# Performance work log

Measured on AMD Instinct MI355X. Metric: run time of the kernel, lower is better.

The kernel has to match this reference:

```python
import jax, jax.numpy as jnp
import numpy as np

B, S, E, H, NQ = 8, 2048, 8, 2, 8
D = E // H  # head_dim = 4
DIM = 2 ** NQ  # 256-amplitude state vector

# CNOT chain pattern from the module: (0,1),(1,2),...,(NQ-2,NQ-1),(NQ-1,0)
CNOTS = [(i, i + 1) for i in range(NQ - 1)] + [(NQ - 1, 0)]

# Pauli-Z sign table: wire 0 is the most-significant qubit axis (torchquantum convention)
_k = np.arange(DIM)
_SIGNS = (1.0 - 2.0 * ((_k[None, :] >> (NQ - 1 - np.arange(NQ))[:, None]) & 1)).astype(np.float32)  # (NQ, DIM)


def _quantum_measure(tok):
    """Batched simulation of the per-token circuit. tok: (N, E) real -> (N, NQ) <Z> values."""
    n = tok.shape[0]
    idx = jnp.arange(NQ) % D
    # encoder RX(tok[w]) then explicit RX(tok[w % head_dim]) on each wire: angles add.
    half = 0.5 * (tok[:, :NQ] + tok[:, idx])  # (N, NQ)
    a0 = jnp.cos(half).astype(jnp.complex64)
    a1 = (-1j) * jnp.sin(half).astype(jnp.complex64)
    qub = jnp.stack([a0, a1], axis=-1)  # (N, NQ, 2) per-qubit states (product state before CNOTs)
    # Kronecker product across the fixed NQ wires
    state = qub[:, 0, :]
    for w in range(1, NQ):
        state = (state[:, :, None] * qub[:, w, None, :]).reshape(n, -1)
    state = state.reshape((n,) + (2,) * NQ)
    # CNOT chain: flip target axis within control=1 block
    for c, t in CNOTS:
        c0 = jax.lax.index_in_dim(state, 0, c + 1, keepdims=True)
        c1 = jnp.flip(jax.lax.index_in_dim(state, 1, c + 1, keepdims=True), axis=t + 1)
        state = jnp.concatenate([c0, c1], axis=c + 1)
    p = (state.real ** 2 + state.imag ** 2).reshape(n, DIM)  # probabilities
    return p @ jnp.asarray(_SIGNS.T)  # (N, NQ) Pauli-Z expectations


def setup_inputs() -> dict:
    key = jax.random.key(0)
    ks = jax.random.split(key, 5)
    sc = 1.0 / np.sqrt(E)
    return {
        "x": jax.random.normal(ks[0], (B, S, E), jnp.float32),
        "Wq": jax.random.normal(ks[1], (E, E), jnp.float32) * sc,
        "Wk": jax.random.normal(ks[2], (E, E), jnp.float32) * sc,
        "Wv": jax.random.normal(ks[3], (E, E), jnp.float32) * sc,
        "Wo": jax.random.normal(ks[4], (E, E), jnp.float32) * sc,
    }


def reference(x, Wq, Wk, Wv, Wo):
    b, s, _ = x.shape
    # nn.Linear(bias=False): y = x @ W^T
    q = jnp.einsum('bse,fe->bsf', x, Wq).reshape(b, s, H, D)
    k = jnp.einsum('bse,fe->bsf', x, Wk).reshape(b, s, H, D)
    v = jnp.einsum('bse,fe->bsf', x, Wv).reshape(b, s, H, D)
    scores = jnp.einsum('bihd,bjhd->bhij', q, k) / jnp.sqrt(jnp.float32(D))
    attn = jax.nn.softmax(scores, axis=-1)  # dropout is identity at inference
    out = jnp.einsum('bhij,bjhd->bihd', attn, v).reshape(b, s, E)
    z = _quantum_measure(out.reshape(-1, E)).reshape(b, s, NQ)  # NQ == E
    return jnp.einsum('bsq,fq->bsf', z, Wo)
```

## Files before the change

kernel.cpp:

```cpp
#include <hip/hip_runtime.h>


#define SS 2048
#define EE 8

extern "C" __global__ __launch_bounds__(256, 4)
void qa_attn5(const float* __restrict__ x, const float* __restrict__ Wq,
              const float* __restrict__ Wk, const float* __restrict__ Wv,
              float* __restrict__ wsD, float4* __restrict__ wsA) {
    __shared__ float wrow[96];
    __shared__ __align__(16) float4 kv4[512];
    __shared__ float rden[3 * 256];
    __shared__ __align__(16) float4 racc[3 * 256];

    const int bid = blockIdx.x;
    const int jw = bid & 7, rt = (bid >> 3) & 7, h = (bid >> 6) & 1, b = bid >> 7;
    const int tid = threadIdx.x, lane = tid & 63, w = tid >> 6;

    if (tid < 96) {
        const int grp = tid >> 5, d = (tid >> 3) & 3, e = tid & 7;
        const float* W = (grp == 0) ? Wq : (grp == 1 ? Wk : Wv);
        float val = W[(h * 4 + d) * EE + e];
        if (grp == 0) val *= 0.72134752044f;
        wrow[tid] = val;
    }
    __syncthreads();

    {
        const int j = jw * 256 + tid;
        const float* xp = x + ((size_t)(b * SS + j)) * EE;
        float xv[8];
        *(float4*)&xv[0] = *(const float4*)xp;
        *(float4*)&xv[4] = *(const float4*)(xp + 4);
        float kk[4], vv[4];
        #pragma unroll
        for (int d = 0; d < 4; ++d) {
            float sk = 0.f, sv = 0.f;
            #pragma unroll
            for (int e = 0; e < 8; ++e) {
                sk += xv[e] * wrow[32 + d * 8 + e];
                sv += xv[e] * wrow[64 + d * 8 + e];
            }
            kk[d] = sk; vv[d] = sv;
        }
        kv4[tid * 2]     = make_float4(kk[0], kk[1], kk[2], kk[3]);
        kv4[tid * 2 + 1] = make_float4(vv[0], vv[1], vv[2], vv[3]);
    }

    float q[4][4];
    const int row0 = rt * 256 + lane;
    #pragma unroll
    for (int m = 0; m < 4; ++m) {
        const float* xp = x + ((size_t)(b * SS + row0 + m * 64)) * EE;
        float xv[8];
        *(float4*)&xv[0] = *(const float4*)xp;
        *(float4*)&xv[4] = *(const float4*)(xp + 4);
        #pragma unroll
        for (int d = 0; d < 4; ++d) {
            float s = 0.f;
            #pragma unroll
            for (int e = 0; e < 8; ++e) s += xv[e] * wrow[d * 8 + e];
            q[m][d] = s;
        }
    }
    __syncthreads();

    float den[4] = {};
    float acc[4][4] = {};
    const int jb = w * 64;
    #pragma unroll 2
    for (int jl = 0; jl < 64; ++jl) {
        const float4 kk = kv4[(jb + jl) * 2];
        const float4 vv = kv4[(jb + jl) * 2 + 1];
        #pragma unroll
        for (int m = 0; m < 4; ++m) {
            const float s = q[m][0] * kk.x + q[m][1] * kk.y
                          + q[m][2] * kk.z + q[m][3] * kk.w;
            const float e = __builtin_amdgcn_exp2f(s);
            den[m] += e;
            acc[m][0] += e * vv.x; acc[m][1] += e * vv.y;
            acc[m][2] += e * vv.z; acc[m][3] += e * vv.w;
        }
    }

    if (w > 0) {
        #pragma unroll
        for (int m = 0; m < 4; ++m) {
            rden[(w - 1) * 256 + lane + m * 64] = den[m];
            racc[(w - 1) * 256 + lane + m * 64] =
                make_float4(acc[m][0], acc[m][1], acc[m][2], acc[m][3]);
        }
    }
    __syncthreads();
    if (w == 0) {
        #pragma unroll
        for (int m = 0; m < 4; ++m) {
            const int r = lane + m * 64;
            float d = den[m] + rden[r] + rden[256 + r] + rden[512 + r];
            float4 a1 = racc[r], a2 = racc[256 + r], a3 = racc[512 + r];
            float4 a = make_float4(acc[m][0] + a1.x + a2.x + a3.x,
                                   acc[m][1] + a1.y + a2.y + a3.y,
                                   acc[m][2] + a1.z + a2.z + a3.z,
                                   acc[m][3] + a1.w + a2.w + a3.w);
            const size_t idx = ((size_t)((b * 2 + h) * 8 + jw)) * SS + row0 + m * 64;
            wsD[idx] = d;
            wsA[idx] = a;
        }
    }
}

extern "C" __global__ __launch_bounds__(256)
void qa_quantum5(const float* __restrict__ wsD, const float4* __restrict__ wsA,
                 const float* __restrict__ Wo, float* __restrict__ out) {
    __shared__ float wo[64];
    const int tid = threadIdx.x;
    if (tid < 64) wo[tid] = Wo[tid];
    __syncthreads();

    const int g = blockIdx.x * 256 + tid;
    const int b = g >> 11, s = g & 2047;

    float tok[8];
    #pragma unroll
    for (int h = 0; h < 2; ++h) {
        float den = 0.f, a0 = 0.f, a1 = 0.f, a2 = 0.f, a3 = 0.f;
        #pragma unroll
        for (int sl = 0; sl < 8; ++sl) {
            const size_t idx = ((size_t)((b * 2 + h) * 8 + sl)) * SS + s;
            den += wsD[idx];
            const float4 p = wsA[idx];
            a0 += p.x; a1 += p.y; a2 += p.z; a3 += p.w;
        }
        const float inv = 1.f / den;
        tok[h * 4 + 0] = a0 * inv; tok[h * 4 + 1] = a1 * inv;
        tok[h * 4 + 2] = a2 * inv; tok[h * 4 + 3] = a3 * inv;
    }

    float c[8];
    #pragma unroll
    for (int ww = 0; ww < 8; ++ww) c[ww] = __cosf(tok[ww] + tok[ww & 3]);

    float z[8];
    float p = 1.f;
    #pragma unroll
    for (int qq = 1; qq < 8; ++qq) { p *= c[qq]; z[qq] = p; }
    z[0] = p;
    #pragma unroll
    for (int qq = 1; qq < 8; ++qq) z[qq] *= c[0];

    float y[8];
    #pragma unroll
    for (int f = 0; f < 8; ++f) {
        float sum = 0.f;
        #pragma unroll
        for (int qq = 0; qq < 8; ++qq) sum += z[qq] * wo[f * 8 + qq];
        y[f] = sum;
    }
    float* op = out + (size_t)g * 8;
    *(float4*)op       = make_float4(y[0], y[1], y[2], y[3]);
    *(float4*)(op + 4) = make_float4(y[4], y[5], y[6], y[7]);
}

extern "C" void kernel_launch(void* const* d_in, const int* in_sizes, int n_in,
                              void* d_out, int out_size, void* d_ws, size_t ws_size,
                              hipStream_t stream) {
    const float* x  = (const float*)d_in[0];
    const float* Wq = (const float*)d_in[1];
    const float* Wk = (const float*)d_in[2];
    const float* Wv = (const float*)d_in[3];
    const float* Wo = (const float*)d_in[4];
    float* out = (float*)d_out;

    float*  wsD = (float*)d_ws;
    float4* wsA = (float4*)((char*)d_ws + (16 * 8 * 2048) * sizeof(float));

    qa_attn5<<<dim3(1024), dim3(256), 0, stream>>>(x, Wq, Wk, Wv, wsD, wsA);
    qa_quantum5<<<dim3(64), dim3(256), 0, stream>>>(wsD, wsA, Wo, out);
}
```

Baseline: 87.03 us.

## Precompute K/V in separate kernel and read via wave-uniform scalar loads

Moves the K/V projection into its own kernel that writes K and V to a global buffer, so the attention kernel no longer recomputes them per block or stages them in LDS. The attention kernel reads K/V with wave-uniform addresses (readfirstlane), which lets the compiler use scalar loads, and it drops a barrier. Key splits double from 8 to 16, giving more blocks and a larger partial-reduction workload in the final kernel. This adds an extra launch and more workspace traffic.

```diff
diff --git a/kernel.cpp b/kernel.cpp
--- a/kernel.cpp
+++ b/kernel.cpp
@@ -4,48 +4,53 @@
 #define SS 2048
 #define EE 8
 
-extern "C" __global__ __launch_bounds__(256, 4)
-void qa_attn5(const float* __restrict__ x, const float* __restrict__ Wq,
-              const float* __restrict__ Wk, const float* __restrict__ Wv,
+extern "C" __global__ __launch_bounds__(256)
+void qa_kv(const float* __restrict__ x, const float* __restrict__ Wk,
+           const float* __restrict__ Wv, float* __restrict__ kvbuf) {
+    __shared__ float wsh[128];
+    const int tid = threadIdx.x;
+    if (tid < 128) wsh[tid] = (tid < 64) ? Wk[tid] : Wv[tid - 64];
+    __syncthreads();
+
+    const int idx = blockIdx.x * 256 + tid;
+    const int j = idx & 2047, h = (idx >> 11) & 1, b = idx >> 12;
+    const float* xp = x + ((size_t)(b * SS + j)) * EE;
+    float xv[8];
+    *(float4*)&xv[0] = *(const float4*)xp;
+    *(float4*)&xv[4] = *(const float4*)(xp + 4);
+    float o[8];
+    #pragma unroll
+    for (int d = 0; d < 4; ++d) {
+        float sk = 0.f, sv = 0.f;
+        #pragma unroll
+        for (int e = 0; e < 8; ++e) {
+            sk += xv[e] * wsh[(h * 4 + d) * 8 + e];
+            sv += xv[e] * wsh[64 + (h * 4 + d) * 8 + e];
+        }
+        o[d] = sk; o[4 + d] = sv;
+    }
+    float* op = kvbuf + (size_t)idx * 8;
+    *(float4*)op       = make_float4(o[0], o[1], o[2], o[3]);
+    *(float4*)(op + 4) = make_float4(o[4], o[5], o[6], o[7]);
+}
+
+extern "C" __global__ __launch_bounds__(256, 6)
+void qa_attn8(const float* __restrict__ x, const float* __restrict__ Wq,
+              const float* __restrict__ kvbuf,
               float* __restrict__ wsD, float4* __restrict__ wsA) {
-    __shared__ float wrow[96];
-    __shared__ __align__(16) float4 kv4[512];
+    __shared__ float wrow[32];
     __shared__ float rden[3 * 256];
     __shared__ __align__(16) float4 racc[3 * 256];
 
     const int bid = blockIdx.x;
-    const int jw = bid & 7, rt = (bid >> 3) & 7, h = (bid >> 6) & 1, b = bid >> 7;
+    const int jw = bid & 15, rt = (bid >> 4) & 7, h = (bid >> 7) & 1, b = bid >> 8;
     const int tid = threadIdx.x, lane = tid & 63, w = tid >> 6;
 
-    if (tid < 96) {
-        const int grp = tid >> 5, d = (tid >> 3) & 3, e = tid & 7;
-        const float* W = (grp == 0) ? Wq : (grp == 1 ? Wk : Wv);
-        float val = W[(h * 4 + d) * EE + e];
-        if (grp == 0) val *= 0.72134752044f;
-        wrow[tid] = val;
+    if (tid < 32) {
+        const int d = (tid >> 3) & 3, e = tid & 7;
+        wrow[tid] = Wq[(h * 4 + d) * EE + e] * 0.72134752044f;
     }
     __syncthreads();
-
-    {
-        const int j = jw * 256 + tid;
-        const float* xp = x + ((size_t)(b * SS + j)) * EE;
-        float xv[8];
-        *(float4*)&xv[0] = *(const float4*)xp;
-        *(float4*)&xv[4] = *(const float4*)(xp + 4);
-        float kk[4], vv[4];
-        #pragma unroll
-        for (int d = 0; d < 4; ++d) {
-            float sk = 0.f, sv = 0.f;
-            #pragma unroll
-            for (int e = 0; e < 8; ++e) {
-                sk += xv[e] * wrow[32 + d * 8 + e];
-                sv += xv[e] * wrow[64 + d * 8 + e];
-            }
-            kk[d] = sk; vv[d] = sv;
-        }
-        kv4[tid * 2]     = make_float4(kk[0], kk[1], kk[2], kk[3]);
-        kv4[tid * 2 + 1] = make_float4(vv[0], vv[1], vv[2], vv[3]);
-    }
 
     float q[4][4];
     const int row0 = rt * 256 + lane;
@@ -63,23 +68,29 @@
             q[m][d] = s;
         }
     }
-    __syncthreads();
+
+    const int wu = __builtin_amdgcn_readfirstlane(w);
+    const float* __restrict__ kvp =
+        kvbuf + (((size_t)((b * 2 + h) * SS)) + jw * 128 + wu * 32) * 8;
 
     float den[4] = {};
     float acc[4][4] = {};
-    const int jb = w * 64;
-    #pragma unroll 2
-    for (int jl = 0; jl < 64; ++jl) {
-        const float4 kk = kv4[(jb + jl) * 2];
-        const float4 vv = kv4[(jb + jl) * 2 + 1];
+    #pragma unroll 4
+    for (int jl = 0; jl < 32; ++jl) {
+        const float k0 = kvp[jl * 8 + 0], k1 = kvp[jl * 8 + 1];
+        const float k2 = kvp[jl * 8 + 2], k3 = kvp[jl * 8 + 3];
+        const float v0 = kvp[jl * 8 + 4], v1 = kvp[jl * 8 + 5];
+        const float v2 = kvp[jl * 8 + 6], v3 = kvp[jl * 8 + 7];
         #pragma unroll
         for (int m = 0; m < 4; ++m) {
-            const float s = q[m][0] * kk.x + q[m][1] * kk.y
-                          + q[m][2] * kk.z + q[m][3] * kk.w;
+            const float s = fmaf(q[m][0], k0, fmaf(q[m][1], k1,
+                            fmaf(q[m][2], k2, q[m][3] * k3)));
             const float e = __builtin_amdgcn_exp2f(s);
             den[m] += e;
-            acc[m][0] += e * vv.x; acc[m][1] += e * vv.y;
-            acc[m][2] += e * vv.z; acc[m][3] += e * vv.w;
+            acc[m][0] = fmaf(e, v0, acc[m][0]);
+            acc[m][1] = fmaf(e, v1, acc[m][1]);
+            acc[m][2] = fmaf(e, v2, acc[m][2]);
+            acc[m][3] = fmaf(e, v3, acc[m][3]);
         }
     }
 
@@ -102,7 +113,7 @@
                                    acc[m][1] + a1.y + a2.y + a3.y,
                                    acc[m][2] + a1.z + a2.z + a3.z,
                                    acc[m][3] + a1.w + a2.w + a3.w);
-            const size_t idx = ((size_t)((b * 2 + h) * 8 + jw)) * SS + row0 + m * 64;
+            const size_t idx = ((size_t)((b * 2 + h) * 16 + jw)) * SS + row0 + m * 64;
             wsD[idx] = d;
             wsA[idx] = a;
         }
@@ -110,7 +121,7 @@
 }
 
 extern "C" __global__ __launch_bounds__(256)
-void qa_quantum5(const float* __restrict__ wsD, const float4* __restrict__ wsA,
+void qa_quantum8(const float* __restrict__ wsD, const float4* __restrict__ wsA,
                  const float* __restrict__ Wo, float* __restrict__ out) {
     __shared__ float wo[64];
     const int tid = threadIdx.x;
@@ -125,8 +136,8 @@
     for (int h = 0; h < 2; ++h) {
         float den = 0.f, a0 = 0.f, a1 = 0.f, a2 = 0.f, a3 = 0.f;
         #pragma unroll
-        for (int sl = 0; sl < 8; ++sl) {
-            const size_t idx = ((size_t)((b * 2 + h) * 8 + sl)) * SS + s;
+        for (int sl = 0; sl < 16; ++sl) {
+            const size_t idx = ((size_t)((b * 2 + h) * 16 + sl)) * SS + s;
             den += wsD[idx];
             const float4 p = wsA[idx];
             a0 += p.x; a1 += p.y; a2 += p.z; a3 += p.w;
@@ -171,9 +182,11 @@
     const float* Wo = (const float*)d_in[4];
     float* out = (float*)d_out;
 
-    float*  wsD = (float*)d_ws;
-    float4* wsA = (float4*)((char*)d_ws + (16 * 8 * 2048) * sizeof(float));
+    float*  kvbuf = (float*)d_ws;
+    float*  wsD   = (float*)((char*)d_ws + (1 << 20));
+    float4* wsA   = (float4*)((char*)d_ws + (3 << 20));
 
-    qa_attn5<<<dim3(1024), dim3(256), 0, stream>>>(x, Wq, Wk, Wv, wsD, wsA);
-    qa_quantum5<<<dim3(64), dim3(256), 0, stream>>>(wsD, wsA, Wo, out);
+    qa_kv<<<dim3(128), dim3(256), 0, stream>>>(x, Wk, Wv, kvbuf);
+    qa_attn8<<<dim3(2048), dim3(256), 0, stream>>>(x, Wq, kvbuf, wsD, wsA);
+    qa_quantum8<<<dim3(64), dim3(256), 0, stream>>>(wsD, wsA, Wo, out);
 }
```

Measured after the change: 90.00 us. 1.03x slower.
